# Kernel tuning notes

Measured on AMD Instinct MI355X. Metric: run time of the kernel, lower is better.

## Reference

```python
import jax, jax.numpy as jnp
import numpy as np

DIM = 512
HID = 1024        # dim * expansion_factor
QK = 128          # query_key_dim
G = 256           # group_size
EPS = 1e-5


def setup_inputs() -> dict:
    key = jax.random.key(0)
    ks = jax.random.split(key, 6)
    x = jax.random.normal(ks[0], (4, 4096, DIM), jnp.float32)
    ln_w = jnp.ones((DIM,), jnp.float32)
    ln_b = jnp.zeros((DIM,), jnp.float32)
    Wh = 0.02 * jax.random.normal(ks[1], (DIM, 2 * HID), jnp.float32)
    bh = jnp.zeros((2 * HID,), jnp.float32)
    Wqk = 0.02 * jax.random.normal(ks[2], (DIM, QK), jnp.float32)
    bqk = jnp.zeros((QK,), jnp.float32)
    gamma = 0.02 * jax.random.normal(ks[3], (4, QK), jnp.float32)  # nn.init.normal_(gamma, std=0.02)
    beta = jnp.zeros((4, QK), jnp.float32)
    Wo = 0.02 * jax.random.normal(ks[4], (HID, DIM), jnp.float32)
    bo = jnp.zeros((DIM,), jnp.float32)
    return {"x": x, "ln_w": ln_w, "ln_b": ln_b, "Wh": Wh, "bh": bh,
            "Wqk": Wqk, "bqk": bqk, "gamma": gamma, "beta": beta,
            "Wo": Wo, "bo": bo}


def reference(x, ln_w, ln_b, Wh, bh, Wqk, bqk, gamma, beta, Wo, bo):
    b, n, _ = x.shape
    g = n // G  # number of groups (n chosen as multiple of G -> no padding)

    # LayerNorm (torch uses biased variance)
    mu = jnp.mean(x, axis=-1, keepdims=True)
    var = jnp.mean((x - mu) ** 2, axis=-1, keepdims=True)
    normed = (x - mu) * jax.lax.rsqrt(var + EPS) * ln_w + ln_b

    # to_hidden: Linear -> SiLU, split into v / gate
    h = jax.nn.silu(normed @ Wh + bh)            # [b, n, 2*HID]
    v, gate = jnp.split(h, 2, axis=-1)           # each [b, n, HID]

    # to_qk: Linear -> SiLU, then 4-head offset/scale
    qk = jax.nn.silu(normed @ Wqk + bqk)         # [b, n, QK]
    qkh = qk[..., None, :] * gamma + beta        # [b, n, 4, QK]
    quad_q, lin_q, quad_k, lin_k = (qkh[..., i, :] for i in range(4))

    # group: b (g n) d -> b g n d
    grp = lambda t: t.reshape(b, g, G, t.shape[-1])
    qq, qk_, lq, lk, vv = map(grp, (quad_q, quad_k, lin_q, lin_k, v))

    # quadratic (group-local) attention with ReLU^2 scores, causal within group
    sim = jnp.einsum('bgid,bgjd->bgij', qq, qk_) / G
    attn = jnp.square(jnp.maximum(sim, 0.0))
    causal_mask = jnp.triu(jnp.ones((G, G), dtype=bool), 1)
    attn = jnp.where(causal_mask, 0.0, attn)
    quad_out = jnp.einsum('bgij,bgje->bgie', attn, vv)   # [b, g, G, HID]

    # linear attention across groups: per-group kv, exclusive cumsum over group dim
    lin_kv = jnp.einsum('bgnd,bgne->bgde', lk, vv) / G   # [b, g, QK, HID]
    lin_kv = jnp.cumsum(lin_kv, axis=1)
    lin_kv = jnp.pad(lin_kv, ((0, 0), (1, 0), (0, 0), (0, 0)))[:, :-1]
    lin_out = jnp.einsum('bgde,bgnd->bgne', lin_kv, lq)  # [b, g, G, HID]

    out = gate * (quad_out.reshape(b, n, HID) + lin_out.reshape(b, n, HID))
    return out @ Wo + bo + x
```

## Files before the change

### kernel.cpp

```cpp
#include <hip/hip_runtime.h>
#include <hip/hip_bf16.h>
#include <math.h>


#define BATCH 4
#define SEQ   4096
#define TROWS 16384
#define DIMD  512
#define HIDD  1024
#define QKD   128
#define GRP   256
#define NGRP  16
#define BGRP  64
#define EPIW  132
#define EPB   130

typedef unsigned short bfraw;
typedef __attribute__((ext_vector_type(8))) short bf16x8;
typedef __attribute__((ext_vector_type(8))) unsigned short u16x8;
typedef __attribute__((ext_vector_type(4))) unsigned int u32x4;
typedef __attribute__((ext_vector_type(4))) float f32x4;

__device__ __forceinline__ float bf2f(bfraw u) {
    union { float f; unsigned int i; } c;
    c.i = ((unsigned int)u) << 16;
    return c.f;
}
__device__ __forceinline__ bfraw f2bf(float f) {
    unsigned int x = __float_as_uint(f);
    unsigned int r = (x + 0x7fffu + ((x >> 16) & 1u)) >> 16;
    return (bfraw)r;
}
__device__ __forceinline__ unsigned int pkbf(float lo, float hi) {
    __hip_bfloat162 h2 = __float22bfloat162_rn(make_float2(lo, hi));
    union { __hip_bfloat162 h; unsigned int u; } c; c.h = h2;
    return c.u;
}
__device__ __forceinline__ void store16bf(bfraw* dst, const float* src) {
    u32x4 a, b;
    #pragma unroll
    for (int k = 0; k < 4; ++k) a[k] = pkbf(src[2 * k], src[2 * k + 1]);
    #pragma unroll
    for (int k = 0; k < 4; ++k) b[k] = pkbf(src[8 + 2 * k], src[8 + 2 * k + 1]);
    *(u32x4*)dst = a;
    *(u32x4*)(dst + 8) = b;
}
__device__ __forceinline__ float silu_f(float z) {
    return z / (1.f + __expf(-z));
}
__device__ __forceinline__ void gload_lds16(const void* g, void* l) {
    __builtin_amdgcn_global_load_lds(
        (const __attribute__((address_space(1))) unsigned int*)g,
        (__attribute__((address_space(3))) unsigned int*)l, 16, 0, 0);
}

__device__ __forceinline__ void mfma_step(const bfraw* As, const bfraw* Bs,
                                          f32x4 acc[4][4], int wm, int wn,
                                          int q, int mi) {
    bf16x8 af[4], bfg[4];
    #pragma unroll
    for (int i = 0; i < 4; ++i)
        af[i] = *(const bf16x8*)&As[(size_t)(wm * 64 + i * 16 + mi) * 32 + q * 8];
    #pragma unroll
    for (int j = 0; j < 4; ++j)
        bfg[j] = *(const bf16x8*)&Bs[(size_t)(wn * 64 + j * 16 + mi) * 32 + q * 8];
    #pragma unroll
    for (int i = 0; i < 4; ++i)
        #pragma unroll
        for (int j = 0; j < 4; ++j)
            acc[i][j] = __builtin_amdgcn_mfma_f32_16x16x32_bf16(af[i], bfg[j], acc[i][j], 0, 0, 0);
}

#define SMEM_DECL(sz)                                           \
    __shared__ __align__(16) char smem_[sz];                    \
    bfraw* As0 = (bfraw*)smem_;                                 \
    bfraw* As1 = (bfraw*)(smem_ + 8192);                        \
    bfraw* Bs0 = (bfraw*)(smem_ + 16384);                       \
    bfraw* Bs1 = (bfraw*)(smem_ + 24576);

#define KLOOP_PRE(Abase, Astr, Bbase, Bstr)                                    \
    const bfraw* pa0 = (Abase) + (size_t)(t >> 2) * (Astr) + (t & 3) * 8;      \
    const bfraw* pa1 = pa0 + (size_t)64 * (Astr);                              \
    const bfraw* pb0 = (Bbase) + (size_t)(t >> 2) * (Bstr) + (t & 3) * 8;      \
    const bfraw* pb1 = pb0 + (size_t)64 * (Bstr);

#define LDS_DSTS                                                               \
    bfraw* lA0  = As0 + (size_t)wid * 512;                                     \
    bfraw* lA0b = As0 + 2048 + (size_t)wid * 512;                              \
    bfraw* lA1  = As1 + (size_t)wid * 512;                                     \
    bfraw* lA1b = As1 + 2048 + (size_t)wid * 512;                              \
    bfraw* lB0  = Bs0 + (size_t)wid * 512;                                     \
    bfraw* lB0b = Bs0 + 2048 + (size_t)wid * 512;                              \
    bfraw* lB1  = Bs1 + (size_t)wid * 512;                                     \
    bfraw* lB1b = Bs1 + 2048 + (size_t)wid * 512;

#define KSTEP64P                                                               \
    do {                                                                       \
        gload_lds16(pa0,      lA0);                                            \
        gload_lds16(pa1,      lA0b);                                           \
        gload_lds16(pa0 + 32, lA1);                                            \
        gload_lds16(pa1 + 32, lA1b);                                           \
        gload_lds16(pb0,      lB0);                                            \
        gload_lds16(pb1,      lB0b);                                           \
        gload_lds16(pb0 + 32, lB1);                                            \
        gload_lds16(pb1 + 32, lB1b);                                           \
        __syncthreads();                                                       \
        mfma_step(As0, Bs0, acc, wm, wn, q, mi);                               \
        mfma_step(As1, Bs1, acc, wm, wn, q, mi);                               \
        __syncthreads();                                                       \
        pa0 += 64; pa1 += 64; pb0 += 64; pb1 += 64;                            \
    } while (0)

__device__ __forceinline__ int epi_row(int p, int lr) {
    return (lr < 16) ? (p * 16 + lr) : (64 + p * 16 + (lr - 16));
}

__global__ __launch_bounds__(256) void ln_kernel(const float* __restrict__ x,
                                                 const float* __restrict__ w,
                                                 const float* __restrict__ b,
                                                 bfraw* __restrict__ outb) {
    int row  = blockIdx.x * 4 + (threadIdx.x >> 6);
    int lane = threadIdx.x & 63;
    const float* xr = x + (size_t)row * DIMD;
    float4 v0 = ((const float4*)xr)[lane];
    float4 v1 = ((const float4*)xr)[lane + 64];
    float s  = v0.x + v0.y + v0.z + v0.w + v1.x + v1.y + v1.z + v1.w;
    float ss = v0.x*v0.x + v0.y*v0.y + v0.z*v0.z + v0.w*v0.w
             + v1.x*v1.x + v1.y*v1.y + v1.z*v1.z + v1.w*v1.w;
    #pragma unroll
    for (int off = 32; off; off >>= 1) {
        s  += __shfl_xor(s, off);
        ss += __shfl_xor(ss, off);
    }
    float mu  = s * (1.f / DIMD);
    float var = ss * (1.f / DIMD) - mu * mu;
    float inv = rsqrtf(var + 1e-5f);
    float4 w0 = ((const float4*)w)[lane],  w1 = ((const float4*)w)[lane + 64];
    float4 b0 = ((const float4*)b)[lane],  b1 = ((const float4*)b)[lane + 64];
    unsigned int o0 = pkbf((v0.x - mu) * inv * w0.x + b0.x,
                           (v0.y - mu) * inv * w0.y + b0.y);
    unsigned int o1 = pkbf((v0.z - mu) * inv * w0.z + b0.z,
                           (v0.w - mu) * inv * w0.w + b0.w);
    unsigned int o2 = pkbf((v1.x - mu) * inv * w1.x + b1.x,
                           (v1.y - mu) * inv * w1.y + b1.y);
    unsigned int o3 = pkbf((v1.z - mu) * inv * w1.z + b1.z,
                           (v1.w - mu) * inv * w1.w + b1.w);
    unsigned int* brow = (unsigned int*)(outb + (size_t)row * DIMD);
    ((uint2*)brow)[lane]      = make_uint2(o0, o1);
    ((uint2*)brow)[lane + 64] = make_uint2(o2, o3);
}

__global__ __launch_bounds__(256) void transpose_f32_bf16(const float* __restrict__ in,
                                                          bfraw* __restrict__ outp,
                                                          int R, int C) {
    __shared__ float tile[32][33];
    int c0 = blockIdx.x * 32, r0 = blockIdx.y * 32;
    int t = threadIdx.x;
    int tr = t >> 3, tc4 = (t & 7) * 4;
    float4 v = *(const float4*)&in[(size_t)(r0 + tr) * C + c0 + tc4];
    tile[tr][tc4 + 0] = v.x; tile[tr][tc4 + 1] = v.y;
    tile[tr][tc4 + 2] = v.z; tile[tr][tc4 + 3] = v.w;
    __syncthreads();
    ushort4 s;
    s.x = f2bf(tile[tc4 + 0][tr]);
    s.y = f2bf(tile[tc4 + 1][tr]);
    s.z = f2bf(tile[tc4 + 2][tr]);
    s.w = f2bf(tile[tc4 + 3][tr]);
    *(ushort4*)&outp[(size_t)(c0 + tr) * R + r0 + tc4] = s;
}

__global__ __launch_bounds__(256) void gemm_h(const bfraw* __restrict__ A,
                                              const bfraw* __restrict__ BT,
                                              const float* __restrict__ bias,
                                              bfraw* __restrict__ vT,
                                              bfraw* __restrict__ gate) {
    SMEM_DECL(33280)
    bfraw* epi2 = (bfraw*)smem_;
    int t = threadIdx.x;
    int lane = t & 63, wid = t >> 6;
    int wm = wid >> 1, wn = wid & 1;
    int q = lane >> 4, mi = lane & 15;
    int row0 = blockIdx.y * 128, col0 = blockIdx.x * 128;
    f32x4 acc[4][4] = {};
    LDS_DSTS
    {
        KLOOP_PRE(A + (size_t)row0 * DIMD, DIMD, BT + (size_t)col0 * DIMD, DIMD)
        #pragma unroll
        for (int k0 = 0; k0 < DIMD; k0 += 64) KSTEP64P;
    }
    #pragma unroll
    for (int p = 0; p < 4; ++p)
        #pragma unroll
        for (int j = 0; j < 4; ++j) {
            float bv = bias[col0 + wn * 64 + j * 16 + mi];
            #pragma unroll
            for (int rg = 0; rg < 4; ++rg) {
                int rowl = wm * 64 + p * 16 + q * 4 + rg;
                epi2[rowl * EPB + wn * 64 + j * 16 + mi] = f2bf(silu_f(acc[p][j][rg] + bv));
            }
        }
    __syncthreads();
    int bg = row0 >> 8;
    if (col0 < HIDD) {
        int e2 = t & 63, jblk = t >> 6;
        const unsigned int* ep32 = (const unsigned int*)epi2;
        unsigned int wv[32];
        #pragma unroll
        for (int jj = 0; jj < 32; ++jj)
            wv[jj] = ep32[(size_t)(jblk * 32 + jj) * 65 + e2];
        int jbase = (row0 & 255) + jblk * 32;
        bfraw* dst0 = vT + ((size_t)bg * HIDD + col0 + 2 * e2) * GRP + jbase;
        bfraw* dst1 = dst0 + GRP;
        #pragma unroll
        for (int vq = 0; vq < 4; ++vq) {
            u16x8 s;
            #pragma unroll
            for (int k = 0; k < 8; ++k) s[k] = (bfraw)(wv[vq * 8 + k] & 0xffffu);
            *(u16x8*)(dst0 + vq * 8) = s;
        }
        #pragma unroll
        for (int vq = 0; vq < 4; ++vq) {
            u16x8 s;
            #pragma unroll
            for (int k = 0; k < 8; ++k) s[k] = (bfraw)(wv[vq * 8 + k] >> 16);
            *(u16x8*)(dst1 + vq * 8) = s;
        }
    } else {
        int lr = t >> 1, seg = t & 1;
        const bfraw* src = epi2 + (size_t)lr * EPB + seg * 64;
        bfraw* dst = gate + (size_t)(row0 + lr) * HIDD + (col0 - HIDD) + seg * 64;
        #pragma unroll
        for (int vq = 0; vq < 8; ++vq)
            *(u16x8*)(dst + vq * 8) = *(const u16x8*)(src + vq * 8);
    }
}

__global__ __launch_bounds__(256) void qk_mfma(const bfraw* __restrict__ A,
                                               const bfraw* __restrict__ BT,
                                               const float* __restrict__ bqk,
                                               const float* __restrict__ gamma,
                                               const float* __restrict__ beta,
                                               bfraw* __restrict__ qq,
                                               bfraw* __restrict__ lq,
                                               bfraw* __restrict__ kk,
                                               bfraw* __restrict__ lkT) {
    SMEM_DECL(32768)
    float* epi = (float*)smem_;
    int t = threadIdx.x;
    int lane = t & 63, wid = t >> 6;
    int wm = wid >> 1, wn = wid & 1;
    int q = lane >> 4, mi = lane & 15;
    int row0 = blockIdx.y * 128;
    f32x4 acc[4][4] = {};
    LDS_DSTS
    {
        KLOOP_PRE(A + (size_t)row0 * DIMD, DIMD, BT, DIMD)
        #pragma unroll
        for (int k0 = 0; k0 < DIMD; k0 += 64) KSTEP64P;
    }
    int bg = row0 >> 8;
    #pragma unroll
    for (int p = 0; p < 4; ++p) {
        #pragma unroll
        for (int j = 0; j < 4; ++j) {
            float bv = bqk[wn * 64 + j * 16 + mi];
            #pragma unroll
            for (int rg = 0; rg < 4; ++rg)
                epi[(wm * 16 + q * 4 + rg) * EPIW + wn * 64 + j * 16 + mi] =
                    silu_f(acc[p][j][rg] + bv);
        }
        __syncthreads();
        {
            int lr = t >> 3, c0t = (t & 7) * 16;
            int gr = row0 + epi_row(p, lr);
            const float* src = &epi[lr * EPIW + c0t];
            float z[16];
            #pragma unroll
            for (int k = 0; k < 16; ++k) z[k] = src[k];
            #pragma unroll
            for (int hd = 0; hd < 3; ++hd) {
                bfraw* arr = (hd == 0) ? qq : (hd == 1) ? lq : kk;
                const float* gp = gamma + hd * QKD + c0t;
                const float* ep = beta  + hd * QKD + c0t;
                float tmp[16];
                #pragma unroll
                for (int k = 0; k < 16; ++k) tmp[k] = z[k] * gp[k] + ep[k];
                store16bf(arr + (size_t)gr * QKD + c0t, tmp);
            }
        }
        {
            int c = t >> 1, half = t & 1;
            float g3 = gamma[3 * QKD + c], e3 = beta[3 * QKD + c];
            int j0 = (row0 & 255) + half * 64 + p * 16;
            float tmp[16];
            #pragma unroll
            for (int k = 0; k < 16; ++k)
                tmp[k] = epi[(half * 16 + k) * EPIW + c] * g3 + e3;
            store16bf(lkT + ((size_t)bg * QKD + c) * GRP + j0, tmp);
        }
        __syncthreads();
    }
}

__global__ __launch_bounds__(256) void sim_mfma(const bfraw* __restrict__ qq,
                                                const bfraw* __restrict__ kk,
                                                bfraw* __restrict__ attn) {
    int bg = blockIdx.y;
    int tid = blockIdx.x;
    int ry = (tid == 0) ? 0 : 1;
    int rx = (tid == 2) ? 1 : 0;
    int row0 = ry * 128, col0 = rx * 128;
    SMEM_DECL(32768)
    float* epi = (float*)smem_;
    int t = threadIdx.x;
    int lane = t & 63, wid = t >> 6;
    int wm = wid >> 1, wn = wid & 1;
    int q = lane >> 4, mi = lane & 15;
    f32x4 acc[4][4] = {};
    LDS_DSTS
    {
        KLOOP_PRE(qq + (size_t)(bg * GRP + row0) * QKD, QKD,
                  kk + (size_t)(bg * GRP + col0) * QKD, QKD)
        #pragma unroll
        for (int k0 = 0; k0 < QKD; k0 += 64) KSTEP64P;
    }
    bfraw* ag = attn + (size_t)bg * GRP * GRP;
    #pragma unroll
    for (int p = 0; p < 4; ++p) {
        #pragma unroll
        for (int j = 0; j < 4; ++j) {
            int colg = col0 + wn * 64 + j * 16 + mi;
            #pragma unroll
            for (int rg = 0; rg < 4; ++rg) {
                int rowg = row0 + wm * 64 + p * 16 + q * 4 + rg;
                float s = acc[p][j][rg] * (1.f / GRP);
                s = fmaxf(s, 0.f);
                s = s * s;
                epi[(wm * 16 + q * 4 + rg) * EPIW + wn * 64 + j * 16 + mi] =
                    (colg > rowg) ? 0.f : s;
            }
        }
        __syncthreads();
        int lr = t >> 3, c0t = (t & 7) * 16;
        int gr = row0 + epi_row(p, lr);
        store16bf(ag + (size_t)gr * GRP + col0 + c0t, &epi[lr * EPIW + c0t]);
        __syncthreads();
    }
}

__global__ __launch_bounds__(256) void kv_mfma(const bfraw* __restrict__ vT,
                                               const bfraw* __restrict__ lkT,
                                               bfraw* __restrict__ kvT_raw) {
    int bg = blockIdx.z;
    int row0 = blockIdx.y * 128;
    SMEM_DECL(32768)
    float* epi = (float*)smem_;
    int t = threadIdx.x;
    int lane = t & 63, wid = t >> 6;
    int wm = wid >> 1, wn = wid & 1;
    int q = lane >> 4, mi = lane & 15;
    f32x4 acc[4][4] = {};
    LDS_DSTS
    {
        KLOOP_PRE(vT + (size_t)bg * HIDD * GRP + (size_t)row0 * GRP, GRP,
                  lkT + (size_t)bg * QKD * GRP, GRP)
        #pragma unroll
        for (int k0 = 0; k0 < GRP; k0 += 64) KSTEP64P;
    }
    bfraw* outg = kvT_raw + (size_t)bg * HIDD * QKD;
    #pragma unroll
    for (int p = 0; p < 4; ++p) {
        #pragma unroll
        for (int j = 0; j < 4; ++j)
            #pragma unroll
            for (int rg = 0; rg < 4; ++rg)
                epi[(wm * 16 + q * 4 + rg) * EPIW + wn * 64 + j * 16 + mi] = acc[p][j][rg];
        __syncthreads();
        int lr = t >> 3, c0t = (t & 7) * 16;
        int gr = row0 + epi_row(p, lr);
        store16bf(outg + (size_t)gr * QKD + c0t, &epi[lr * EPIW + c0t]);
        __syncthreads();
    }
}

__global__ __launch_bounds__(256) void cumsum2_kernel(const bfraw* __restrict__ raw,
                                                      bfraw* __restrict__ ex) {
    int idx = blockIdx.x * 256 + threadIdx.x;
    int b = idx >> 17;
    int r = idx & 131071;
    const bfraw* rp = raw + (size_t)b * NGRP * 131072 + r;
    bfraw* ep = ex + (size_t)b * NGRP * 131072 + r;
    float run = 0.f;
    #pragma unroll
    for (int g = 0; g < NGRP; ++g) {
        ep[(size_t)g * 131072] = f2bf(run);
        run += bf2f(rp[(size_t)g * 131072]) * (1.f / GRP);
    }
}

__global__ __launch_bounds__(256) void quadlin_mfma(const bfraw* __restrict__ attn,
                                                    const bfraw* __restrict__ vT,
                                                    const bfraw* __restrict__ lq,
                                                    const bfraw* __restrict__ kvT_ex,
                                                    const bfraw* __restrict__ gate,
                                                    bfraw* __restrict__ gated) {
    int bg = blockIdx.z;
    int row0 = blockIdx.y * 128;
    int col0 = blockIdx.x * 128;
    SMEM_DECL(32768)
    float* epi = (float*)smem_;
    int t = threadIdx.x;
    int lane = t & 63, wid = t >> 6;
    int wm = wid >> 1, wn = wid & 1;
    int q = lane >> 4, mi = lane & 15;
    f32x4 acc[4][4] = {};
    LDS_DSTS
    {
        KLOOP_PRE(attn + (size_t)bg * GRP * GRP + (size_t)row0 * GRP, GRP,
                  vT + (size_t)bg * HIDD * GRP + (size_t)col0 * GRP, GRP)
        int kmax = row0 + 128;
        for (int k0 = 0; k0 < kmax; k0 += 64) KSTEP64P;
    }
    {
        KLOOP_PRE(lq + (size_t)(bg * GRP + row0) * QKD, QKD,
                  kvT_ex + (size_t)bg * HIDD * QKD + (size_t)col0 * QKD, QKD)
        #pragma unroll
        for (int k0 = 0; k0 < QKD; k0 += 64) KSTEP64P;
    }
    #pragma unroll
    for (int p = 0; p < 4; ++p) {
        #pragma unroll
        for (int j = 0; j < 4; ++j)
            #pragma unroll
            for (int rg = 0; rg < 4; ++rg)
                epi[(wm * 16 + q * 4 + rg) * EPIW + wn * 64 + j * 16 + mi] = acc[p][j][rg];
        __syncthreads();
        int lr = t >> 3, c0t = (t & 7) * 16;
        int gr = row0 + epi_row(p, lr);
        size_t grow = (size_t)bg * GRP + gr;
        const float* src = &epi[lr * EPIW + c0t];
        const bfraw* gsrc = gate + grow * HIDD + col0 + c0t;
        u16x8 g0 = *(const u16x8*)gsrc;
        u16x8 g1 = *(const u16x8*)(gsrc + 8);
        float tmp[16];
        #pragma unroll
        for (int k = 0; k < 8; ++k) tmp[k] = src[k] * bf2f(g0[k]);
        #pragma unroll
        for (int k = 0; k < 8; ++k) tmp[8 + k] = src[8 + k] * bf2f(g1[k]);
        store16bf(gated + grow * HIDD + col0 + c0t, tmp);
        __syncthreads();
    }
}

__global__ __launch_bounds__(256) void gemm_final(const bfraw* __restrict__ A,
                                                  const bfraw* __restrict__ BT,
                                                  const float* __restrict__ bo,
                                                  const float* __restrict__ x,
                                                  float* __restrict__ out) {
    SMEM_DECL(32768)
    float* epi = (float*)smem_;
    int t = threadIdx.x;
    int lane = t & 63, wid = t >> 6;
    int wm = wid >> 1, wn = wid & 1;
    int q = lane >> 4, mi = lane & 15;
    int row0 = blockIdx.y * 128, col0 = blockIdx.x * 128;
    f32x4 acc[4][4] = {};
    LDS_DSTS
    {
        KLOOP_PRE(A + (size_t)row0 * HIDD, HIDD, BT + (size_t)col0 * HIDD, HIDD)
        #pragma unroll
        for (int k0 = 0; k0 < HIDD; k0 += 64) KSTEP64P;
    }
    #pragma unroll
    for (int p = 0; p < 4; ++p) {
        #pragma unroll
        for (int j = 0; j < 4; ++j) {
            float bv = bo[col0 + wn * 64 + j * 16 + mi];
            #pragma unroll
            for (int rg = 0; rg < 4; ++rg)
                epi[(wm * 16 + q * 4 + rg) * EPIW + wn * 64 + j * 16 + mi] =
                    acc[p][j][rg] + bv;
        }
        __syncthreads();
        int lr = t >> 3, c0t = (t & 7) * 16;
        int gr = row0 + epi_row(p, lr);
        const float* src = &epi[lr * EPIW + c0t];
        const float* xsrc = x + (size_t)gr * DIMD + col0 + c0t;
        float* dst = out + (size_t)gr * DIMD + col0 + c0t;
        #pragma unroll
        for (int v = 0; v < 4; ++v) {
            float4 a = ((const float4*)src)[v];
            float4 xv = ((const float4*)xsrc)[v];
            a.x += xv.x; a.y += xv.y; a.z += xv.z; a.w += xv.w;
            ((float4*)dst)[v] = a;
        }
        __syncthreads();
    }
}

extern "C" void kernel_launch(void* const* d_in, const int* in_sizes, int n_in,
                              void* d_out, int out_size, void* d_ws, size_t ws_size,
                              hipStream_t stream) {
    const float* x     = (const float*)d_in[0];
    const float* ln_w  = (const float*)d_in[1];
    const float* ln_b  = (const float*)d_in[2];
    const float* Wh    = (const float*)d_in[3];
    const float* bh    = (const float*)d_in[4];
    const float* Wqk   = (const float*)d_in[5];
    const float* bqk   = (const float*)d_in[6];
    const float* gamma = (const float*)d_in[7];
    const float* beta  = (const float*)d_in[8];
    const float* Wo    = (const float*)d_in[9];
    const float* bo    = (const float*)d_in[10];
    float* out = (float*)d_out;

    char* outb_ = (char*)d_out;
    bfraw* attn = (bfraw*)(outb_);
    bfraw* qq   = (bfraw*)(outb_ + 8388608);
    bfraw* kk   = (bfraw*)(outb_ + 12582912);
    bfraw* lq   = (bfraw*)(outb_ + 16777216);
    bfraw* WhT  = (bfraw*)(outb_ + 20971520);
    bfraw* WqkT = (bfraw*)(outb_ + 23068672);

    char* wsb = (char*)d_ws;
    bfraw* vT      = (bfraw*)(wsb);
    bfraw* gate    = (bfraw*)(wsb + 33554432);
    bfraw* gated   = (bfraw*)(wsb + 67108864);
    bfraw* normb   = (bfraw*)(wsb + 100663296);
    bfraw* kvT_raw = (bfraw*)(wsb + 117440512);
    bfraw* kvT_ex  = (bfraw*)(wsb + 134217728);
    bfraw* lkT     = (bfraw*)(wsb + 150994944);
    bfraw* WoT     = (bfraw*)(wsb + 155189248);

    transpose_f32_bf16<<<dim3(2 * HIDD / 32, DIMD / 32), 256, 0, stream>>>(Wh, WhT, DIMD, 2 * HIDD);
    transpose_f32_bf16<<<dim3(DIMD / 32, HIDD / 32), 256, 0, stream>>>(Wo, WoT, HIDD, DIMD);
    transpose_f32_bf16<<<dim3(QKD / 32, DIMD / 32), 256, 0, stream>>>(Wqk, WqkT, DIMD, QKD);
    ln_kernel<<<TROWS / 4, 256, 0, stream>>>(x, ln_w, ln_b, normb);
    gemm_h<<<dim3(2 * HIDD / 128, TROWS / 128), 256, 0, stream>>>(normb, WhT, bh, vT, gate);
    qk_mfma<<<dim3(1, TROWS / 128), 256, 0, stream>>>(normb, WqkT, bqk, gamma, beta, qq, lq, kk, lkT);
    sim_mfma<<<dim3(3, BGRP), 256, 0, stream>>>(qq, kk, attn);
    kv_mfma<<<dim3(1, HIDD / 128, BGRP), 256, 0, stream>>>(vT, lkT, kvT_raw);
    cumsum2_kernel<<<(BATCH * QKD * HIDD) / 256, 256, 0, stream>>>(kvT_raw, kvT_ex);
    quadlin_mfma<<<dim3(HIDD / 128, GRP / 128, BGRP), 256, 0, stream>>>(
        attn, vT, lq, kvT_ex, gate, gated);
    gemm_final<<<dim3(DIMD / 128, TROWS / 128), 256, 0, stream>>>(gated, WoT, bo, x, out);
}
```

Before: 296.3 us.

## Widen GEMM tiles to 128x256 and compute vT directly as transposed GEMM

Introduces a 128x256 MFMA tile path (each wave computes a 64x128 sub-tile) and uses it for the gate GEMM, the quad/linear attention GEMM and the final output GEMM, raising arithmetic intensity per block. The hidden projection is split into two kernels: the v half is computed as WhT x normb per group, so the output is already in vT layout and the in-LDS transpose epilogue is no longer needed. The larger tiles use 48KB LDS and more accumulator registers, and halve the block count, which can reduce occupancy and tail balance.

```diff
diff --git a/kernel.cpp b/kernel.cpp
--- a/kernel.cpp
+++ b/kernel.cpp
@@ -13,7 +13,7 @@
 #define NGRP  16
 #define BGRP  64
 #define EPIW  132
-#define EPB   130
+#define EP2W  260
 
 typedef unsigned short bfraw;
 typedef __attribute__((ext_vector_type(8))) short bf16x8;
@@ -115,6 +115,73 @@
     return (lr < 16) ? (p * 16 + lr) : (64 + p * 16 + (lr - 16));
 }
 
+__device__ __forceinline__ void mfma_step256(const bfraw* As, const bfraw* Bs,
+                                             f32x4 acc[4][8], int wr, int wc,
+                                             int q, int mi) {
+    bf16x8 af[4], bfg[8];
+    #pragma unroll
+    for (int i = 0; i < 4; ++i)
+        af[i] = *(const bf16x8*)&As[(size_t)(wr * 64 + i * 16 + mi) * 32 + q * 8];
+    #pragma unroll
+    for (int j = 0; j < 8; ++j)
+        bfg[j] = *(const bf16x8*)&Bs[(size_t)(wc * 128 + j * 16 + mi) * 32 + q * 8];
+    #pragma unroll
+    for (int i = 0; i < 4; ++i)
+        #pragma unroll
+        for (int j = 0; j < 8; ++j)
+            acc[i][j] = __builtin_amdgcn_mfma_f32_16x16x32_bf16(af[i], bfg[j], acc[i][j], 0, 0, 0);
+}
+
+#define SMEM256_DECL                                            \
+    __shared__ __align__(16) char smem_[49152];                 \
+    bfraw* As0 = (bfraw*)smem_;                                 \
+    bfraw* As1 = (bfraw*)(smem_ + 8192);                        \
+    bfraw* Bs0 = (bfraw*)(smem_ + 16384);                       \
+    bfraw* Bs1 = (bfraw*)(smem_ + 32768);
+
+#define KPRE256(Abase, Astr, Bbase, Bstr)                                      \
+    const bfraw* pa0 = (Abase) + (size_t)(t >> 2) * (Astr) + (t & 3) * 8;      \
+    const bfraw* pa1 = pa0 + (size_t)64 * (Astr);                              \
+    const bfraw* pb0 = (Bbase) + (size_t)(t >> 2) * (Bstr) + (t & 3) * 8;      \
+    const bfraw* pb1 = pb0 + (size_t)64 * (Bstr);                              \
+    const bfraw* pb2 = pb0 + (size_t)128 * (Bstr);                             \
+    const bfraw* pb3 = pb0 + (size_t)192 * (Bstr);
+
+#define LDS256_DSTS                                                            \
+    bfraw* lA0  = As0 + (size_t)wid * 512;                                     \
+    bfraw* lA0b = As0 + 2048 + (size_t)wid * 512;                              \
+    bfraw* lA1  = As1 + (size_t)wid * 512;                                     \
+    bfraw* lA1b = As1 + 2048 + (size_t)wid * 512;                              \
+    bfraw* lB00 = Bs0 + (size_t)wid * 512;                                     \
+    bfraw* lB01 = Bs0 + 2048 + (size_t)wid * 512;                              \
+    bfraw* lB02 = Bs0 + 4096 + (size_t)wid * 512;                              \
+    bfraw* lB03 = Bs0 + 6144 + (size_t)wid * 512;                              \
+    bfraw* lB10 = Bs1 + (size_t)wid * 512;                                     \
+    bfraw* lB11 = Bs1 + 2048 + (size_t)wid * 512;                              \
+    bfraw* lB12 = Bs1 + 4096 + (size_t)wid * 512;                              \
+    bfraw* lB13 = Bs1 + 6144 + (size_t)wid * 512;
+
+#define KSTEP64W                                                               \
+    do {                                                                       \
+        gload_lds16(pa0,      lA0);                                            \
+        gload_lds16(pa1,      lA0b);                                           \
+        gload_lds16(pa0 + 32, lA1);                                            \
+        gload_lds16(pa1 + 32, lA1b);                                           \
+        gload_lds16(pb0,      lB00);                                           \
+        gload_lds16(pb1,      lB01);                                           \
+        gload_lds16(pb2,      lB02);                                           \
+        gload_lds16(pb3,      lB03);                                           \
+        gload_lds16(pb0 + 32, lB10);                                           \
+        gload_lds16(pb1 + 32, lB11);                                           \
+        gload_lds16(pb2 + 32, lB12);                                           \
+        gload_lds16(pb3 + 32, lB13);                                           \
+        __syncthreads();                                                       \
+        mfma_step256(As0, Bs0, acc, wr, wc, q, mi);                            \
+        mfma_step256(As1, Bs1, acc, wr, wc, q, mi);                            \
+        __syncthreads();                                                       \
+        pa0 += 64; pa1 += 64; pb0 += 64; pb1 += 64; pb2 += 64; pb3 += 64;      \
+    } while (0)
+
 __global__ __launch_bounds__(256) void ln_kernel(const float* __restrict__ x,
                                                  const float* __restrict__ w,
                                                  const float* __restrict__ b,
@@ -169,69 +236,86 @@
     *(ushort4*)&outp[(size_t)(c0 + tr) * R + r0 + tc4] = s;
 }
 
-__global__ __launch_bounds__(256) void gemm_h(const bfraw* __restrict__ A,
-                                              const bfraw* __restrict__ BT,
-                                              const float* __restrict__ bias,
-                                              bfraw* __restrict__ vT,
-                                              bfraw* __restrict__ gate) {
-    SMEM_DECL(33280)
-    bfraw* epi2 = (bfraw*)smem_;
+__global__ __launch_bounds__(256, 2) void gemm_vT(const bfraw* __restrict__ WhTv,
+                                                  const bfraw* __restrict__ normb,
+                                                  const float* __restrict__ bias,
+                                                  bfraw* __restrict__ vT) {
+    SMEM256_DECL
+    float* epi = (float*)smem_;
     int t = threadIdx.x;
     int lane = t & 63, wid = t >> 6;
-    int wm = wid >> 1, wn = wid & 1;
+    int wr = wid & 1, wc = wid >> 1;
     int q = lane >> 4, mi = lane & 15;
-    int row0 = blockIdx.y * 128, col0 = blockIdx.x * 128;
-    f32x4 acc[4][4] = {};
-    LDS_DSTS
-    {
-        KLOOP_PRE(A + (size_t)row0 * DIMD, DIMD, BT + (size_t)col0 * DIMD, DIMD)
-        #pragma unroll
-        for (int k0 = 0; k0 < DIMD; k0 += 64) KSTEP64P;
-    }
-    #pragma unroll
-    for (int p = 0; p < 4; ++p)
-        #pragma unroll
-        for (int j = 0; j < 4; ++j) {
-            float bv = bias[col0 + wn * 64 + j * 16 + mi];
-            #pragma unroll
-            for (int rg = 0; rg < 4; ++rg) {
-                int rowl = wm * 64 + p * 16 + q * 4 + rg;
-                epi2[rowl * EPB + wn * 64 + j * 16 + mi] = f2bf(silu_f(acc[p][j][rg] + bv));
-            }
-        }
-    __syncthreads();
-    int bg = row0 >> 8;
-    if (col0 < HIDD) {
-        int e2 = t & 63, jblk = t >> 6;
-        const unsigned int* ep32 = (const unsigned int*)epi2;
-        unsigned int wv[32];
-        #pragma unroll
-        for (int jj = 0; jj < 32; ++jj)
-            wv[jj] = ep32[(size_t)(jblk * 32 + jj) * 65 + e2];
-        int jbase = (row0 & 255) + jblk * 32;
-        bfraw* dst0 = vT + ((size_t)bg * HIDD + col0 + 2 * e2) * GRP + jbase;
-        bfraw* dst1 = dst0 + GRP;
-        #pragma unroll
-        for (int vq = 0; vq < 4; ++vq) {
-            u16x8 s;
-            #pragma unroll
-            for (int k = 0; k < 8; ++k) s[k] = (bfraw)(wv[vq * 8 + k] & 0xffffu);
-            *(u16x8*)(dst0 + vq * 8) = s;
-        }
-        #pragma unroll
-        for (int vq = 0; vq < 4; ++vq) {
-            u16x8 s;
-            #pragma unroll
-            for (int k = 0; k < 8; ++k) s[k] = (bfraw)(wv[vq * 8 + k] >> 16);
-            *(u16x8*)(dst1 + vq * 8) = s;
-        }
-    } else {
-        int lr = t >> 1, seg = t & 1;
-        const bfraw* src = epi2 + (size_t)lr * EPB + seg * 64;
-        bfraw* dst = gate + (size_t)(row0 + lr) * HIDD + (col0 - HIDD) + seg * 64;
-        #pragma unroll
-        for (int vq = 0; vq < 8; ++vq)
-            *(u16x8*)(dst + vq * 8) = *(const u16x8*)(src + vq * 8);
+    int row0 = blockIdx.y * 128;
+    int bg = blockIdx.z;
+    f32x4 acc[4][8] = {};
+    LDS256_DSTS
+    {
+        KPRE256(WhTv + (size_t)row0 * DIMD, DIMD,
+                normb + (size_t)bg * GRP * DIMD, DIMD)
+        #pragma unroll
+        for (int k0 = 0; k0 < DIMD; k0 += 64) KSTEP64W;
+    }
+    bfraw* outg = vT + (size_t)bg * HIDD * GRP;
+    #pragma unroll
+    for (int p = 0; p < 4; ++p) {
+        #pragma unroll
+        for (int rg = 0; rg < 4; ++rg) {
+            float bv = bias[row0 + wr * 64 + p * 16 + q * 4 + rg];
+            #pragma unroll
+            for (int j = 0; j < 8; ++j)
+                epi[(wr * 16 + q * 4 + rg) * EP2W + wc * 128 + j * 16 + mi] =
+                    silu_f(acc[p][j][rg] + bv);
+        }
+        __syncthreads();
+        int lr = t >> 3;
+        int gr = row0 + epi_row(p, lr);
+        #pragma unroll
+        for (int half = 0; half < 2; ++half) {
+            int c0t = (t & 7) * 16 + half * 128;
+            store16bf(outg + (size_t)gr * GRP + c0t, &epi[lr * EP2W + c0t]);
+        }
+        __syncthreads();
+    }
+}
+
+__global__ __launch_bounds__(256, 2) void gemm_gate(const bfraw* __restrict__ A,
+                                                    const bfraw* __restrict__ BT,
+                                                    const float* __restrict__ bias,
+                                                    bfraw* __restrict__ gate) {
+    SMEM256_DECL
+    float* epi = (float*)smem_;
+    int t = threadIdx.x;
+    int lane = t & 63, wid = t >> 6;
+    int wr = wid & 1, wc = wid >> 1;
+    int q = lane >> 4, mi = lane & 15;
+    int row0 = blockIdx.y * 128, col0 = blockIdx.x * 256;
+    f32x4 acc[4][8] = {};
+    LDS256_DSTS
+    {
+        KPRE256(A + (size_t)row0 * DIMD, DIMD, BT + (size_t)col0 * DIMD, DIMD)
+        #pragma unroll
+        for (int k0 = 0; k0 < DIMD; k0 += 64) KSTEP64W;
+    }
+    #pragma unroll
+    for (int p = 0; p < 4; ++p) {
+        #pragma unroll
+        for (int j = 0; j < 8; ++j) {
+            float bv = bias[col0 + wc * 128 + j * 16 + mi];
+            #pragma unroll
+            for (int rg = 0; rg < 4; ++rg)
+                epi[(wr * 16 + q * 4 + rg) * EP2W + wc * 128 + j * 16 + mi] =
+                    silu_f(acc[p][j][rg] + bv);
+        }
+        __syncthreads();
+        int lr = t >> 3;
+        int gr = row0 + epi_row(p, lr);
+        #pragma unroll
+        for (int half = 0; half < 2; ++half) {
+            int c0t = (t & 7) * 16 + half * 128;
+            store16bf(gate + (size_t)gr * HIDD + col0 + c0t, &epi[lr * EP2W + c0t]);
+        }
+        __syncthreads();
     }
 }
 
@@ -398,101 +482,109 @@
     }
 }
 
-__global__ __launch_bounds__(256) void quadlin_mfma(const bfraw* __restrict__ attn,
-                                                    const bfraw* __restrict__ vT,
-                                                    const bfraw* __restrict__ lq,
-                                                    const bfraw* __restrict__ kvT_ex,
-                                                    const bfraw* __restrict__ gate,
-                                                    bfraw* __restrict__ gated) {
+__global__ __launch_bounds__(256, 2) void quadlin_mfma(const bfraw* __restrict__ attn,
+                                                       const bfraw* __restrict__ vT,
+                                                       const bfraw* __restrict__ lq,
+                                                       const bfraw* __restrict__ kvT_ex,
+                                                       const bfraw* __restrict__ gate,
+                                                       bfraw* __restrict__ gated) {
     int bg = blockIdx.z;
     int row0 = blockIdx.y * 128;
-    int col0 = blockIdx.x * 128;
-    SMEM_DECL(32768)
+    int col0 = blockIdx.x * 256;
+    SMEM256_DECL
     float* epi = (float*)smem_;
     int t = threadIdx.x;
     int lane = t & 63, wid = t >> 6;
-    int wm = wid >> 1, wn = wid & 1;
+    int wr = wid & 1, wc = wid >> 1;
     int q = lane >> 4, mi = lane & 15;
-    f32x4 acc[4][4] = {};
-    LDS_DSTS
-    {
-        KLOOP_PRE(attn + (size_t)bg * GRP * GRP + (size_t)row0 * GRP, GRP,
-                  vT + (size_t)bg * HIDD * GRP + (size_t)col0 * GRP, GRP)
+    f32x4 acc[4][8] = {};
+    LDS256_DSTS
+    {
+        KPRE256(attn + (size_t)bg * GRP * GRP + (size_t)row0 * GRP, GRP,
+                vT + (size_t)bg * HIDD * GRP + (size_t)col0 * GRP, GRP)
         int kmax = row0 + 128;
-        for (int k0 = 0; k0 < kmax; k0 += 64) KSTEP64P;
-    }
-    {
-        KLOOP_PRE(lq + (size_t)(bg * GRP + row0) * QKD, QKD,
-                  kvT_ex + (size_t)bg * HIDD * QKD + (size_t)col0 * QKD, QKD)
-        #pragma unroll
-        for (int k0 = 0; k0 < QKD; k0 += 64) KSTEP64P;
+        for (int k0 = 0; k0 < kmax; k0 += 64) KSTEP64W;
+    }
+    {
+        KPRE256(lq + (size_t)(bg * GRP + row0) * QKD, QKD,
+                kvT_ex + (size_t)bg * HIDD * QKD + (size_t)col0 * QKD, QKD)
+        #pragma unroll
+        for (int k0 = 0; k0 < QKD; k0 += 64) KSTEP64W;
     }
     #pragma unroll
     for (int p = 0; p < 4; ++p) {
         #pragma unroll
-        for (int j = 0; j < 4; ++j)
+        for (int j = 0; j < 8; ++j)
             #pragma unroll
             for (int rg = 0; rg < 4; ++rg)
-                epi[(wm * 16 + q * 4 + rg) * EPIW + wn * 64 + j * 16 + mi] = acc[p][j][rg];
-        __syncthreads();
-        int lr = t >> 3, c0t = (t & 7) * 16;
+                epi[(wr * 16 + q * 4 + rg) * EP2W + wc * 128 + j * 16 + mi] = acc[p][j][rg];
+        __syncthreads();
+        int lr = t >> 3;
         int gr = row0 + epi_row(p, lr);
         size_t grow = (size_t)bg * GRP + gr;
-        const float* src = &epi[lr * EPIW + c0t];
-        const bfraw* gsrc = gate + grow * HIDD + col0 + c0t;
-        u16x8 g0 = *(const u16x8*)gsrc;
-        u16x8 g1 = *(const u16x8*)(gsrc + 8);
-        float tmp[16];
-        #pragma unroll
-        for (int k = 0; k < 8; ++k) tmp[k] = src[k] * bf2f(g0[k]);
-        #pragma unroll
-        for (int k = 0; k < 8; ++k) tmp[8 + k] = src[8 + k] * bf2f(g1[k]);
-        store16bf(gated + grow * HIDD + col0 + c0t, tmp);
-        __syncthreads();
-    }
-}
-
-__global__ __launch_bounds__(256) void gemm_final(const bfraw* __restrict__ A,
-                                                  const bfraw* __restrict__ BT,
-                                                  const float* __restrict__ bo,
-                                                  const float* __restrict__ x,
-                                                  float* __restrict__ out) {
-    SMEM_DECL(32768)
+        #pragma unroll
+        for (int half = 0; half < 2; ++half) {
+            int c0t = (t & 7) * 16 + half * 128;
+            const float* src = &epi[lr * EP2W + c0t];
+            const bfraw* gsrc = gate + grow * HIDD + col0 + c0t;
+            u16x8 g0 = *(const u16x8*)gsrc;
+            u16x8 g1 = *(const u16x8*)(gsrc + 8);
+            float tmp[16];
+            #pragma unroll
+            for (int k = 0; k < 8; ++k) tmp[k] = src[k] * bf2f(g0[k]);
+            #pragma unroll
+            for (int k = 0; k < 8; ++k) tmp[8 + k] = src[8 + k] * bf2f(g1[k]);
+            store16bf(gated + grow * HIDD + col0 + c0t, tmp);
+        }
+        __syncthreads();
+    }
+}
+
+__global__ __launch_bounds__(256, 2) void gemm_final(const bfraw* __restrict__ A,
+                                                     const bfraw* __restrict__ BT,
+                                                     const float* __restrict__ bo,
+                                                     const float* __restrict__ x,
+                                                     float* __restrict__ out) {
+    SMEM256_DECL
     float* epi = (float*)smem_;
     int t = threadIdx.x;
     int lane = t & 63, wid = t >> 6;
-    int wm = wid >> 1, wn = wid & 1;
+    int wr = wid & 1, wc = wid >> 1;
     int q = lane >> 4, mi = lane & 15;
-    int row0 = blockIdx.y * 128, col0 = blockIdx.x * 128;
-    f32x4 acc[4][4] = {};
-    LDS_DSTS
-    {
-        KLOOP_PRE(A + (size_t)row0 * HIDD, HIDD, BT + (size_t)col0 * HIDD, HIDD)
-        #pragma unroll
-        for (int k0 = 0; k0 < HIDD; k0 += 64) KSTEP64P;
+    int row0 = blockIdx.y * 128, col0 = blockIdx.x * 256;
+    f32x4 acc[4][8] = {};
+    LDS256_DSTS
+    {
+        KPRE256(A + (size_t)row0 * HIDD, HIDD, BT + (size_t)col0 * HIDD, HIDD)
+        #pragma unroll
+        for (int k0 = 0; k0 < HIDD; k0 += 64) KSTEP64W;
     }
     #pragma unroll
     for (int p = 0; p < 4; ++p) {
         #pragma unroll
-        for (int j = 0; j < 4; ++j) {
-            float bv = bo[col0 + wn * 64 + j * 16 + mi];
+        for (int j = 0; j < 8; ++j) {
+            float bv = bo[col0 + wc * 128 + j * 16 + mi];
             #pragma unroll
             for (int rg = 0; rg < 4; ++rg)
-                epi[(wm * 16 + q * 4 + rg) * EPIW + wn * 64 + j * 16 + mi] =
+                epi[(wr * 16 + q * 4 + rg) * EP2W + wc * 128 + j * 16 + mi] =
                     acc[p][j][rg] + bv;
         }
         __syncthreads();
-        int lr = t >> 3, c0t = (t & 7) * 16;
+        int lr = t >> 3;
         int gr = row0 + epi_row(p, lr);
-        const float* src = &epi[lr * EPIW + c0t];
-        const float* xsrc = x + (size_t)gr * DIMD + col0 + c0t;
-        float* dst = out + (size_t)gr * DIMD + col0 + c0t;
-        #pragma unroll
-        for (int v = 0; v < 4; ++v) {
-            float4 a = ((const float4*)src)[v];
-            float4 xv = ((const float4*)xsrc)[v];
-            a.x += xv.x; a.y += xv.y; a.z += xv.z; a.w += xv.w;
-            ((float4*)dst)[v] = a;
+        #pragma unroll
+        for (int half = 0; half < 2; ++half) {
+            int c0t = (t & 7) * 16 + half * 128;
+            const float* src = &epi[lr * EP2W + c0t];
+            const float* xsrc = x + (size_t)gr * DIMD + col0 + c0t;
+            float* dst = out + (size_t)gr * DIMD + col0 + c0t;
+            #pragma unroll
+            for (int v = 0; v < 4; ++v) {
+                float4 a = ((const float4*)src)[v];
+                float4 xv = ((const float4*)xsrc)[v];
+                a.x += xv.x; a.y += xv.y; a.z += xv.z; a.w += xv.w;
+                ((float4*)dst)[v] = a;
+            }
         }
         __syncthreads();
     }
@@ -536,12 +628,14 @@
     transpose_f32_bf16<<<dim3(DIMD / 32, HIDD / 32), 256, 0, stream>>>(Wo, WoT, HIDD, DIMD);
     transpose_f32_bf16<<<dim3(QKD / 32, DIMD / 32), 256, 0, stream>>>(Wqk, WqkT, DIMD, QKD);
     ln_kernel<<<TROWS / 4, 256, 0, stream>>>(x, ln_w, ln_b, normb);
-    gemm_h<<<dim3(2 * HIDD / 128, TROWS / 128), 256, 0, stream>>>(normb, WhT, bh, vT, gate);
+    gemm_vT<<<dim3(1, HIDD / 128, BGRP), 256, 0, stream>>>(WhT, normb, bh, vT);
+    gemm_gate<<<dim3(HIDD / 256, TROWS / 128), 256, 0, stream>>>(
+        normb, WhT + (size_t)HIDD * DIMD, bh + HIDD, gate);
     qk_mfma<<<dim3(1, TROWS / 128), 256, 0, stream>>>(normb, WqkT, bqk, gamma, beta, qq, lq, kk, lkT);
     sim_mfma<<<dim3(3, BGRP), 256, 0, stream>>>(qq, kk, attn);
     kv_mfma<<<dim3(1, HIDD / 128, BGRP), 256, 0, stream>>>(vT, lkT, kvT_raw);
     cumsum2_kernel<<<(BATCH * QKD * HIDD) / 256, 256, 0, stream>>>(kvT_raw, kvT_ex);
-    quadlin_mfma<<<dim3(HIDD / 128, GRP / 128, BGRP), 256, 0, stream>>>(
+    quadlin_mfma<<<dim3(HIDD / 256, GRP / 128, BGRP), 256, 0, stream>>>(
         attn, vT, lq, kvT_ex, gate, gated);
-    gemm_final<<<dim3(DIMD / 128, TROWS / 128), 256, 0, stream>>>(gated, WoT, bo, x, out);
-}
+    gemm_final<<<dim3(DIMD / 256, TROWS / 128), 256, 0, stream>>>(gated, WoT, bo, x, out);
+}
```

Measured after the change: 306.5 us. 3.4% more time.
